# Kernel tuning notes

Measured on AMD Instinct MI355X. Metric: run time of the kernel, lower is better.

## Reference

```python
import jax, jax.numpy as jnp
import numpy as np

Z_SIZE = 32  # latent dimensionality (z_size)


def setup_inputs() -> dict:
    key = jax.random.key(0)
    B, T = 4, 512
    # `mapped` = output of the 1d-conv encoder net: [B, T, 3*z_size]
    mapped = jax.random.uniform(key, (B, T, 3 * Z_SIZE), dtype=jnp.float32)
    return {"mapped": mapped}


def reference(mapped):
    B, T, C = mapped.shape
    z = C // 3
    # transpose last two dims: [B, 3z, T]
    mt = jnp.transpose(mapped, (0, 2, 1))
    mapped_mean = mt[:, :z]                      # [B, z, T]
    covar = mt[:, z:].reshape(B, z, 2 * T)       # [B, z, 2T]
    vals = covar[:, :, :-1]                      # [B, z, 2T-1]
    v_diag = vals[:, :, :T]                      # main diagonal values
    v_super = vals[:, :, T:]                     # superdiagonal values (T-1)
    # Build dense upper-bidiagonal precision cholesky: diag = v+1 (eye added), super = v_super
    i = jnp.arange(T)
    prec_tril = jnp.zeros((B, z, T, T), dtype=mapped.dtype)
    prec_tril = prec_tril.at[:, :, i, i].set(v_diag + 1.0)
    prec_tril = prec_tril.at[:, :, i[:-1], i[1:]].set(v_super)
    eye = jnp.broadcast_to(jnp.eye(T, dtype=mapped.dtype), prec_tril.shape)
    # cov_tril = prec_tril^{-1} via upper-triangular solve against identity
    cov_tril = jax.scipy.linalg.solve_triangular(prec_tril, eye, lower=False)
    cov_tril = jnp.where(jnp.isfinite(cov_tril), cov_tril, jnp.zeros_like(cov_tril))
    # lower-triangular scale factor: transpose last two dims
    cov_tril_lower = jnp.swapaxes(cov_tril, -1, -2)  # [B, z, T, T]
    # (original wraps these in MultivariateNormalTriL(loc=mapped_mean, scale_tril=cov_tril_lower))
    return (mapped_mean, cov_tril_lower)
```

## Files before the change

kernel.cpp:

```cpp
#include <hip/hip_runtime.h>
#include <math.h>

#define BB 4
#define TT 512
#define ZZ 32
#define CC 96
#define NSLICE (BB * ZZ)

__global__ __launch_bounds__(512) void prep_kernel(const float* __restrict__ mapped,
                                                   float* __restrict__ out_mean,
                                                   float* __restrict__ dinv,
                                                   float* __restrict__ Lpre) {
    const int slice = blockIdx.x;
    const int b = slice >> 5;
    const int z = slice & 31;
    const int t = threadIdx.x;

    const float* row = mapped + ((size_t)b * TT + t) * CC;
    const float meanv = row[z];
    const float dval  = row[ZZ + 2 * z] + 1.0f;
    const float sval  = (t < TT - 1) ? row[ZZ + 2 * z + 1] : 0.0f;

    out_mean[slice * TT + t] = meanv;
    const float di = 1.0f / dval;
    dinv[slice * TT + t] = di;

    float g = 0.0f;
    if (t < TT - 1) g = fmaxf(log2f(sval * di), -200.0f);

    __shared__ float sh[TT];
    sh[t] = g;
    __syncthreads();
    #pragma unroll
    for (int off = 1; off < TT; off <<= 1) {
        float v = (t >= off) ? sh[t - off] : 0.0f;
        __syncthreads();
        sh[t] += v;
        __syncthreads();
    }
    const float L = (t == 0) ? 0.0f : sh[t - 1];
    Lpre[slice * TT + t] = L;
}

__global__ __launch_bounds__(256) void fill_kernel(const float* __restrict__ dinv,
                                                   const float* __restrict__ Lpre,
                                                   float* __restrict__ out_tril) {
    const int gid = blockIdx.x * 256 + threadIdx.x;
    const int slice = gid >> 16;
    const int rem = gid & 65535;
    const int i  = rem >> 7;
    const int j4 = (rem & 127) << 2;

    const float* Ls = Lpre + slice * TT;
    const float Li = Ls[i];
    const float di = dinv[slice * TT + i];
    const float4 Lj = *reinterpret_cast<const float4*>(Ls + j4);

    float4 o;
    {
        const int j = j4 + 0;
        if (j > i) o.x = 0.0f;
        else { float r = exp2f(Li - Lj.x) * di; o.x = ((i - j) & 1) ? -r : r; }
    }
    {
        const int j = j4 + 1;
        if (j > i) o.y = 0.0f;
        else { float r = exp2f(Li - Lj.y) * di; o.y = ((i - j) & 1) ? -r : r; }
    }
    {
        const int j = j4 + 2;
        if (j > i) o.z = 0.0f;
        else { float r = exp2f(Li - Lj.z) * di; o.z = ((i - j) & 1) ? -r : r; }
    }
    {
        const int j = j4 + 3;
        if (j > i) o.w = 0.0f;
        else { float r = exp2f(Li - Lj.w) * di; o.w = ((i - j) & 1) ? -r : r; }
    }
    reinterpret_cast<float4*>(out_tril)[gid] = o;
}

extern "C" void kernel_launch(void* const* d_in, const int* in_sizes, int n_in,
                              void* d_out, int out_size, void* d_ws, size_t ws_size,
                              hipStream_t stream) {
    const float* mapped = (const float*)d_in[0];
    float* out = (float*)d_out;

    float* out_mean = out;
    float* out_tril = out + NSLICE * TT;

    float* dinv = (float*)d_ws;
    float* Lpre = dinv + NSLICE * TT;

    prep_kernel<<<NSLICE, TT, 0, stream>>>(mapped, out_mean, dinv, Lpre);

    const int n_f4 = NSLICE * TT * TT / 4;
    fill_kernel<<<n_f4 / 256, 256, 0, stream>>>(dinv, Lpre, out_tril);
}
```

Before: 136.3 us.

## Use wave-shuffle scan, raw exp2 and nontemporal stores in tril fill

The prefix-sum in the prep kernel moves from a shared-memory Hillis-Steele scan with many barriers to a wavefront shuffle scan plus a small cross-wave combine. The fill kernel now computes branch-free with the raw hardware exp2 intrinsic and a precomputed sign parity. It writes the large output with nontemporal vector stores to avoid cache pollution. The output write of about 134 MB dominates, so the compute changes matter mainly if the kernel is not fully bandwidth bound. The raw exp2 may differ slightly for denormal or extreme inputs.

```diff
diff --git a/kernel.cpp b/kernel.cpp
--- a/kernel.cpp
+++ b/kernel.cpp
@@ -6,6 +6,9 @@
 #define ZZ 32
 #define CC 96
 #define NSLICE (BB * ZZ)
+
+typedef float vf4 __attribute__((ext_vector_type(4)));
+
 
 __global__ __launch_bounds__(512) void prep_kernel(const float* __restrict__ mapped,
                                                    float* __restrict__ out_mean,
@@ -28,18 +31,23 @@
     float g = 0.0f;
     if (t < TT - 1) g = fmaxf(log2f(sval * di), -200.0f);
 
-    __shared__ float sh[TT];
-    sh[t] = g;
+    const int lane = t & 63;
+    const int wid  = t >> 6;
+    float v = g;
+    #pragma unroll
+    for (int off = 1; off < 64; off <<= 1) {
+        float n = __shfl_up(v, off, 64);
+        if (lane >= off) v += n;
+    }
+    __shared__ float wsum[8];
+    if (lane == 63) wsum[wid] = v;
     __syncthreads();
+    float offv = 0.0f;
     #pragma unroll
-    for (int off = 1; off < TT; off <<= 1) {
-        float v = (t >= off) ? sh[t - off] : 0.0f;
-        __syncthreads();
-        sh[t] += v;
-        __syncthreads();
-    }
-    const float L = (t == 0) ? 0.0f : sh[t - 1];
-    Lpre[slice * TT + t] = L;
+    for (int w = 0; w < 8; ++w)
+        if (w < wid) offv += wsum[w];
+    const float incl = v + offv;
+    Lpre[slice * TT + t] = incl - g;
 }
 
 __global__ __launch_bounds__(256) void fill_kernel(const float* __restrict__ dinv,
@@ -51,33 +59,35 @@
     const int i  = rem >> 7;
     const int j4 = (rem & 127) << 2;
 
-    const float* Ls = Lpre + slice * TT;
+    const float* Ls = Lpre + (slice << 9);
     const float Li = Ls[i];
-    const float di = dinv[slice * TT + i];
-    const float4 Lj = *reinterpret_cast<const float4*>(Ls + j4);
+    const float di = dinv[(slice << 9) + i];
+    const vf4 Lj = *reinterpret_cast<const vf4*>(Ls + j4);
 
-    float4 o;
+    const int p0 = i & 1;
+
+    vf4 o;
     {
-        const int j = j4 + 0;
-        if (j > i) o.x = 0.0f;
-        else { float r = exp2f(Li - Lj.x) * di; o.x = ((i - j) & 1) ? -r : r; }
+        float r = __builtin_amdgcn_exp2f(Li - Lj.x) * di;
+        r = p0 ? -r : r;
+        o.x = (j4 + 0 <= i) ? r : 0.0f;
     }
     {
-        const int j = j4 + 1;
-        if (j > i) o.y = 0.0f;
-        else { float r = exp2f(Li - Lj.y) * di; o.y = ((i - j) & 1) ? -r : r; }
+        float r = __builtin_amdgcn_exp2f(Li - Lj.y) * di;
+        r = p0 ? r : -r;
+        o.y = (j4 + 1 <= i) ? r : 0.0f;
     }
     {
-        const int j = j4 + 2;
-        if (j > i) o.z = 0.0f;
-        else { float r = exp2f(Li - Lj.z) * di; o.z = ((i - j) & 1) ? -r : r; }
+        float r = __builtin_amdgcn_exp2f(Li - Lj.z) * di;
+        r = p0 ? -r : r;
+        o.z = (j4 + 2 <= i) ? r : 0.0f;
     }
     {
-        const int j = j4 + 3;
-        if (j > i) o.w = 0.0f;
-        else { float r = exp2f(Li - Lj.w) * di; o.w = ((i - j) & 1) ? -r : r; }
+        float r = __builtin_amdgcn_exp2f(Li - Lj.w) * di;
+        r = p0 ? r : -r;
+        o.w = (j4 + 3 <= i) ? r : 0.0f;
     }
-    reinterpret_cast<float4*>(out_tril)[gid] = o;
+    __builtin_nontemporal_store(o, reinterpret_cast<vf4*>(out_tril) + gid);
 }
 
 extern "C" void kernel_launch(void* const* d_in, const int* in_sizes, int n_in,
```

Result: slower. 139.1 us (+2.1%).
